# Performance work log

Measured on AMD Instinct MI355X. Metric: run time of the kernel, lower is better.

## Reference

```python
import jax, jax.numpy as jnp
import numpy as np

B, T, H = 32, 2048, 512
D = 2 * H  # bidirectional encoder feature dim


def setup_inputs() -> dict:
    key = jax.random.key(0)
    k1, k2, k3, k4, k5 = jax.random.split(key, 5)
    stdv = 1.0 / np.sqrt(H)
    return {
        "hidden": jax.random.normal(k1, (B, D), dtype=jnp.float32),
        "encoder_outputs": jax.random.normal(k2, (B, T, D), dtype=jnp.float32),
        "W_attn": jax.random.normal(k3, (H, 2 * D), dtype=jnp.float32) * stdv,
        "b_attn": jax.random.normal(k4, (H,), dtype=jnp.float32) * stdv,
        "v": jax.random.normal(k5, (H,), dtype=jnp.float32) * stdv,
    }


def reference(hidden, encoder_outputs, W_attn, b_attn, v):
    # The original per-timestep sliding-window loop recomputes a position-wise
    # Linear+tanh+dot whose value is independent of the window index, and
    # overlapping writes overwrite with identical values. The exact same math
    # is full additive attention over all T positions.
    d = encoder_outputs.shape[-1]
    Wh = W_attn[:, :d]   # acts on repeated decoder hidden state
    We = W_attn[:, d:]   # acts on encoder outputs
    # [B, H] ; avoids materializing the [B, T, 4H] concat
    hid_proj = jnp.einsum('bd,hd->bh', hidden, Wh)
    # [B, T, H]
    energy = jnp.tanh(jnp.einsum('btd,hd->bth', encoder_outputs, We)
                      + hid_proj[:, None, :] + b_attn)
    scores = jnp.einsum('bth,h->bt', energy, v)  # [B, T]
    return jax.nn.softmax(scores, axis=1)[:, None, :]  # [B, 1, T]
```

## Files before the change

### kernel.cpp

```cpp
#include <hip/hip_runtime.h>

#define Bv 32
#define Tv 2048
#define Hv 512
#define Dv 1024

using bf16x8 = __attribute__((ext_vector_type(8))) __bf16;
using bf16x4 = __attribute__((ext_vector_type(4))) __bf16;
using f32x4  = __attribute__((ext_vector_type(4))) float;

__global__ void swizzle_we(const float* __restrict__ W, bf16x8* __restrict__ We_sw) {
    int g = blockIdx.x * 256 + threadIdx.x;
    int h = g >> 7;
    int d = (g & 127) * 8;
    const float* src = W + h * (2 * Dv) + Dv + d;
    float4 f0 = *(const float4*)src;
    float4 f1 = *(const float4*)(src + 4);
    bf16x8 o;
    o[0] = (__bf16)f0.x; o[1] = (__bf16)f0.y; o[2] = (__bf16)f0.z; o[3] = (__bf16)f0.w;
    o[4] = (__bf16)f1.x; o[5] = (__bf16)f1.y; o[6] = (__bf16)f1.z; o[7] = (__bf16)f1.w;
    int s = ((h >> 4) * 32 + (d >> 5)) * 64 + (((d >> 3) & 3) << 4) + (h & 15);
    We_sw[s] = o;
}

__global__ void hid_proj_kernel(const float* __restrict__ hidden,
                                const float* __restrict__ W,
                                const float* __restrict__ b_attn,
                                float* __restrict__ hp) {
    int h   = blockIdx.x;
    int tid = threadIdx.x;
    float4 wh = ((const float4*)(W + h * (2 * Dv)))[tid];
    __shared__ float red[4][Bv];
    int lane = tid & 63, w = tid >> 6;
    for (int b = 0; b < Bv; ++b) {
        float4 x = ((const float4*)(hidden + b * Dv))[tid];
        float p = wh.x * x.x + wh.y * x.y + wh.z * x.z + wh.w * x.w;
#pragma unroll
        for (int m = 1; m < 64; m <<= 1) p += __shfl_xor(p, m);
        if (lane == 0) red[w][b] = p;
    }
    __syncthreads();
    if (tid < Bv)
        hp[tid * Hv + h] = red[0][tid] + red[1][tid] + red[2][tid] + red[3][tid] + b_attn[h];
}

__device__ __forceinline__ float fast_tanh(float x) {
    float xc = fminf(fmaxf(x, -9.0f), 9.0f);
    float e  = __expf(2.0f * xc);
    return 1.0f - 2.0f / (e + 1.0f);
}

__global__ __launch_bounds__(512) void attn_main(
    const float* __restrict__ enc, const bf16x8* __restrict__ Bg,
    const float* __restrict__ hp, const float* __restrict__ vvec,
    float* __restrict__ scores)
{
    __shared__ __align__(16) __bf16 Abuf[2][64 * 72];
    __shared__ float redbuf[8][64];

    const int tid   = threadIdx.x;
    const int lane  = tid & 63;
    const int w     = tid >> 6;
    const int row0  = blockIdx.x * 64;
    const int batch = row0 >> 11;

    const int srow = tid >> 3;
    const int sd0  = (tid & 7) * 4;
    const float* gA = enc + (row0 + srow) * Dv + sd0;
    __bf16* lw0 = &Abuf[0][srow * 72 + sd0];

    const bf16x8* Bptr = Bg + (w * 4 * 32) * 64 + lane;

    f32x4 acc[4][4];
#pragma unroll
    for (int i = 0; i < 4; ++i)
#pragma unroll
        for (int j = 0; j < 4; ++j)
            acc[i][j] = (f32x4){0.f, 0.f, 0.f, 0.f};

    float4 f0 = *(const float4*)gA;
    float4 f1 = *(const float4*)(gA + 32);
    bf16x8 Bc[2][4];
#pragma unroll
    for (int ktl = 0; ktl < 2; ++ktl)
#pragma unroll
        for (int j = 0; j < 4; ++j)
            Bc[ktl][j] = Bptr[(j * 32 + ktl) * 64];

    const int arow  = lane & 15;
    const int acol8 = (lane >> 4) * 8;

    for (int kc = 0; kc < 16; ++kc) {
        __bf16* p = lw0 + (kc & 1) * (64 * 72);
        bf16x4 o0, o1;
        o0[0] = (__bf16)f0.x; o0[1] = (__bf16)f0.y; o0[2] = (__bf16)f0.z; o0[3] = (__bf16)f0.w;
        o1[0] = (__bf16)f1.x; o1[1] = (__bf16)f1.y; o1[2] = (__bf16)f1.z; o1[3] = (__bf16)f1.w;
        *(bf16x4*)p        = o0;
        *(bf16x4*)(p + 32) = o1;
        if (kc < 15) {
            f0 = *(const float4*)(gA + (kc + 1) * 64);
            f1 = *(const float4*)(gA + (kc + 1) * 64 + 32);
        }
        __syncthreads();

        bf16x8 Bn[2][4];
        if (kc < 15) {
#pragma unroll
            for (int ktl = 0; ktl < 2; ++ktl)
#pragma unroll
                for (int j = 0; j < 4; ++j)
                    Bn[ktl][j] = Bptr[(j * 32 + (kc + 1) * 2 + ktl) * 64];
        }

        const __bf16* rb = &Abuf[kc & 1][0];
#pragma unroll
        for (int ktl = 0; ktl < 2; ++ktl) {
            bf16x8 a0 = *(const bf16x8*)(rb + (0 * 16 + arow) * 72 + ktl * 32 + acol8);
            bf16x8 a1 = *(const bf16x8*)(rb + (1 * 16 + arow) * 72 + ktl * 32 + acol8);
            bf16x8 a2 = *(const bf16x8*)(rb + (2 * 16 + arow) * 72 + ktl * 32 + acol8);
            bf16x8 a3 = *(const bf16x8*)(rb + (3 * 16 + arow) * 72 + ktl * 32 + acol8);
#pragma unroll
            for (int j = 0; j < 4; ++j) {
                acc[0][j] = __builtin_amdgcn_mfma_f32_16x16x32_bf16(a0, Bc[ktl][j], acc[0][j], 0, 0, 0);
                acc[1][j] = __builtin_amdgcn_mfma_f32_16x16x32_bf16(a1, Bc[ktl][j], acc[1][j], 0, 0, 0);
                acc[2][j] = __builtin_amdgcn_mfma_f32_16x16x32_bf16(a2, Bc[ktl][j], acc[2][j], 0, 0, 0);
                acc[3][j] = __builtin_amdgcn_mfma_f32_16x16x32_bf16(a3, Bc[ktl][j], acc[3][j], 0, 0, 0);
            }
        }
#pragma unroll
        for (int ktl = 0; ktl < 2; ++ktl)
#pragma unroll
            for (int j = 0; j < 4; ++j)
                Bc[ktl][j] = Bn[ktl][j];
    }

    float hpv[4], vv[4];
#pragma unroll
    for (int j = 0; j < 4; ++j) {
        int n  = w * 64 + j * 16 + (lane & 15);
        hpv[j] = hp[batch * Hv + n];
        vv[j]  = vvec[n];
    }
    const int qrow = (lane >> 4) * 4;
#pragma unroll
    for (int mt = 0; mt < 4; ++mt)
#pragma unroll
        for (int r = 0; r < 4; ++r) {
            float p = 0.f;
#pragma unroll
            for (int j = 0; j < 4; ++j)
                p += vv[j] * fast_tanh(acc[mt][j][r] + hpv[j]);
            p += __shfl_xor(p, 1);
            p += __shfl_xor(p, 2);
            p += __shfl_xor(p, 4);
            p += __shfl_xor(p, 8);
            if ((lane & 15) == 0)
                redbuf[w][mt * 16 + qrow + r] = p;
        }
    __syncthreads();
    if (tid < 64) {
        float s = 0.f;
#pragma unroll
        for (int ww = 0; ww < 8; ++ww) s += redbuf[ww][tid];
        scores[row0 + tid] = s;
    }
}

__global__ void softmax_kernel(const float* __restrict__ scores, float* __restrict__ out) {
    int b   = blockIdx.x;
    int tid = threadIdx.x;
    const float* s = scores + b * Tv;
    float local[8];
    float m = -1e30f;
#pragma unroll
    for (int i = 0; i < 8; ++i) { local[i] = s[tid + i * 256]; m = fmaxf(m, local[i]); }
    __shared__ float red[4];
    int lane = tid & 63, w = tid >> 6;
#pragma unroll
    for (int x = 1; x < 64; x <<= 1) m = fmaxf(m, __shfl_xor(m, x));
    if (lane == 0) red[w] = m;
    __syncthreads();
    m = fmaxf(fmaxf(red[0], red[1]), fmaxf(red[2], red[3]));
    float sum = 0.f;
#pragma unroll
    for (int i = 0; i < 8; ++i) { local[i] = expf(local[i] - m); sum += local[i]; }
#pragma unroll
    for (int x = 1; x < 64; x <<= 1) sum += __shfl_xor(sum, x);
    __syncthreads();
    if (lane == 0) red[w] = sum;
    __syncthreads();
    sum = red[0] + red[1] + red[2] + red[3];
    float inv = 1.0f / sum;
#pragma unroll
    for (int i = 0; i < 8; ++i) out[b * Tv + tid + i * 256] = local[i] * inv;
}

extern "C" void kernel_launch(void* const* d_in, const int* in_sizes, int n_in,
                              void* d_out, int out_size, void* d_ws, size_t ws_size,
                              hipStream_t stream) {
    const float* hidden = (const float*)d_in[0];
    const float* enc    = (const float*)d_in[1];
    const float* W      = (const float*)d_in[2];
    const float* b_attn = (const float*)d_in[3];
    const float* v      = (const float*)d_in[4];
    float* out = (float*)d_out;

    char* ws = (char*)d_ws;
    bf16x8* We_sw = (bf16x8*)ws;
    float*  hp    = (float*)(ws + (1 << 20));
    float*  sc    = (float*)(ws + (1 << 20) + (1 << 16));

    swizzle_we<<<256, 256, 0, stream>>>(W, We_sw);
    hid_proj_kernel<<<Hv, 256, 0, stream>>>(hidden, W, b_attn, hp);
    attn_main<<<(Bv * Tv) / 64, 512, 0, stream>>>(enc, We_sw, hp, v, sc);
    softmax_kernel<<<Bv, 256, 0, stream>>>(sc, out);
}
```

Before: 443.2 us.

## Fuse prep kernels, swizzle A tile in LDS, deepen global prefetch, set occupancy

Merges the W_e swizzle and hidden-projection kernels into one launch to save a kernel launch. In the main GEMM, the A tile is stored in LDS in an MFMA-fragment-swizzled layout so each lane reads one contiguous bf16x8. Global loads of encoder rows are prefetched two k-chunks ahead, and the k loop is fully unrolled. The block barrier becomes a raw s_waitcnt lgkmcnt(0)+s_barrier, and launch_bounds asks for 2 blocks per CU, which caps register use and risks spills.

```diff
diff --git a/kernel.cpp b/kernel.cpp
--- a/kernel.cpp
+++ b/kernel.cpp
@@ -9,39 +9,38 @@
 using bf16x4 = __attribute__((ext_vector_type(4))) __bf16;
 using f32x4  = __attribute__((ext_vector_type(4))) float;
 
-__global__ void swizzle_we(const float* __restrict__ W, bf16x8* __restrict__ We_sw) {
-    int g = blockIdx.x * 256 + threadIdx.x;
-    int h = g >> 7;
-    int d = (g & 127) * 8;
-    const float* src = W + h * (2 * Dv) + Dv + d;
-    float4 f0 = *(const float4*)src;
-    float4 f1 = *(const float4*)(src + 4);
-    bf16x8 o;
-    o[0] = (__bf16)f0.x; o[1] = (__bf16)f0.y; o[2] = (__bf16)f0.z; o[3] = (__bf16)f0.w;
-    o[4] = (__bf16)f1.x; o[5] = (__bf16)f1.y; o[6] = (__bf16)f1.z; o[7] = (__bf16)f1.w;
-    int s = ((h >> 4) * 32 + (d >> 5)) * 64 + (((d >> 3) & 3) << 4) + (h & 15);
-    We_sw[s] = o;
-}
-
-__global__ void hid_proj_kernel(const float* __restrict__ hidden,
-                                const float* __restrict__ W,
-                                const float* __restrict__ b_attn,
-                                float* __restrict__ hp) {
-    int h   = blockIdx.x;
-    int tid = threadIdx.x;
-    float4 wh = ((const float4*)(W + h * (2 * Dv)))[tid];
-    __shared__ float red[4][Bv];
-    int lane = tid & 63, w = tid >> 6;
-    for (int b = 0; b < Bv; ++b) {
-        float4 x = ((const float4*)(hidden + b * Dv))[tid];
-        float p = wh.x * x.x + wh.y * x.y + wh.z * x.z + wh.w * x.w;
-#pragma unroll
-        for (int m = 1; m < 64; m <<= 1) p += __shfl_xor(p, m);
-        if (lane == 0) red[w][b] = p;
-    }
-    __syncthreads();
-    if (tid < Bv)
-        hp[tid * Hv + h] = red[0][tid] + red[1][tid] + red[2][tid] + red[3][tid] + b_attn[h];
+__global__ void prep_kernel(const float* __restrict__ W, bf16x8* __restrict__ We_sw,
+                            const float* __restrict__ hidden,
+                            const float* __restrict__ b_attn, float* __restrict__ hp) {
+    if (blockIdx.x < 256) {
+        int g = blockIdx.x * 256 + threadIdx.x;
+        int h = g >> 7;
+        int d = (g & 127) * 8;
+        const float* src = W + h * (2 * Dv) + Dv + d;
+        float4 f0 = *(const float4*)src;
+        float4 f1 = *(const float4*)(src + 4);
+        bf16x8 o;
+        o[0] = (__bf16)f0.x; o[1] = (__bf16)f0.y; o[2] = (__bf16)f0.z; o[3] = (__bf16)f0.w;
+        o[4] = (__bf16)f1.x; o[5] = (__bf16)f1.y; o[6] = (__bf16)f1.z; o[7] = (__bf16)f1.w;
+        int s = ((h >> 4) * 32 + (d >> 5)) * 64 + (((d >> 3) & 3) << 4) + (h & 15);
+        We_sw[s] = o;
+    } else {
+        int h   = blockIdx.x - 256;
+        int tid = threadIdx.x;
+        float4 wh = ((const float4*)(W + h * (2 * Dv)))[tid];
+        __shared__ float red[4][Bv];
+        int lane = tid & 63, w = tid >> 6;
+        for (int b = 0; b < Bv; ++b) {
+            float4 x = ((const float4*)(hidden + b * Dv))[tid];
+            float p = wh.x * x.x + wh.y * x.y + wh.z * x.z + wh.w * x.w;
+#pragma unroll
+            for (int m = 1; m < 64; m <<= 1) p += __shfl_xor(p, m);
+            if (lane == 0) red[w][b] = p;
+        }
+        __syncthreads();
+        if (tid < Bv)
+            hp[tid * Hv + h] = red[0][tid] + red[1][tid] + red[2][tid] + red[3][tid] + b_attn[h];
+    }
 }
 
 __device__ __forceinline__ float fast_tanh(float x) {
@@ -50,12 +49,12 @@
     return 1.0f - 2.0f / (e + 1.0f);
 }
 
-__global__ __launch_bounds__(512) void attn_main(
+__global__ __launch_bounds__(512, 2) void attn_main(
     const float* __restrict__ enc, const bf16x8* __restrict__ Bg,
     const float* __restrict__ hp, const float* __restrict__ vvec,
     float* __restrict__ scores)
 {
-    __shared__ __align__(16) __bf16 Abuf[2][64 * 72];
+    __shared__ bf16x8 Abuf[2][512];
     __shared__ float redbuf[8][64];
 
     const int tid   = threadIdx.x;
@@ -64,12 +63,14 @@
     const int row0  = blockIdx.x * 64;
     const int batch = row0 >> 11;
 
-    const int srow = tid >> 3;
-    const int sd0  = (tid & 7) * 4;
-    const float* gA = enc + (row0 + srow) * Dv + sd0;
-    __bf16* lw0 = &Abuf[0][srow * 72 + sd0];
-
-    const bf16x8* Bptr = Bg + (w * 4 * 32) * 64 + lane;
+    const int srow = tid >> 4;
+    const int kk   = (tid & 15) * 4;
+    const float* gA = enc + (row0 + srow) * Dv + kk;
+    const int mt0  = srow >> 4, aa = srow & 15;
+    const int ktl0 = kk >> 5,  qq = (kk >> 3) & 3, jb = kk & 7;
+    __bf16* lw = (__bf16*)(&Abuf[0][0]) + (((mt0 * 2 + ktl0) * 64 + aa * 4 + qq) << 3) + jb;
+
+    const bf16x8* Bptr = Bg + (w * 128) * 64 + lane;
 
     f32x4 acc[4][4];
 #pragma unroll
@@ -78,8 +79,10 @@
         for (int j = 0; j < 4; ++j)
             acc[i][j] = (f32x4){0.f, 0.f, 0.f, 0.f};
 
-    float4 f0 = *(const float4*)gA;
-    float4 f1 = *(const float4*)(gA + 32);
+    float4 fa0 = *(const float4*)gA;
+    float4 fa1 = *(const float4*)(gA + 32 * Dv);
+    float4 fb0 = *(const float4*)(gA + 64);
+    float4 fb1 = *(const float4*)(gA + 32 * Dv + 64);
     bf16x8 Bc[2][4];
 #pragma unroll
     for (int ktl = 0; ktl < 2; ++ktl)
@@ -87,22 +90,24 @@
         for (int j = 0; j < 4; ++j)
             Bc[ktl][j] = Bptr[(j * 32 + ktl) * 64];
 
-    const int arow  = lane & 15;
-    const int acol8 = (lane >> 4) * 8;
-
+    const int rsl = ((lane & 15) << 2) + (lane >> 4);
+
+#pragma unroll
     for (int kc = 0; kc < 16; ++kc) {
-        __bf16* p = lw0 + (kc & 1) * (64 * 72);
+        __bf16* p = lw + (kc & 1) * 4096;
         bf16x4 o0, o1;
-        o0[0] = (__bf16)f0.x; o0[1] = (__bf16)f0.y; o0[2] = (__bf16)f0.z; o0[3] = (__bf16)f0.w;
-        o1[0] = (__bf16)f1.x; o1[1] = (__bf16)f1.y; o1[2] = (__bf16)f1.z; o1[3] = (__bf16)f1.w;
-        *(bf16x4*)p        = o0;
-        *(bf16x4*)(p + 32) = o1;
-        if (kc < 15) {
-            f0 = *(const float4*)(gA + (kc + 1) * 64);
-            f1 = *(const float4*)(gA + (kc + 1) * 64 + 32);
-        }
-        __syncthreads();
-
+        o0[0] = (__bf16)fa0.x; o0[1] = (__bf16)fa0.y; o0[2] = (__bf16)fa0.z; o0[3] = (__bf16)fa0.w;
+        o1[0] = (__bf16)fa1.x; o1[1] = (__bf16)fa1.y; o1[2] = (__bf16)fa1.z; o1[3] = (__bf16)fa1.w;
+        *(bf16x4*)p          = o0;
+        *(bf16x4*)(p + 2048) = o1;
+
+        asm volatile("s_waitcnt lgkmcnt(0)\n\ts_barrier" ::: "memory");
+
+        fa0 = fb0; fa1 = fb1;
+        if (kc < 14) {
+            fb0 = *(const float4*)(gA + (kc + 2) * 64);
+            fb1 = *(const float4*)(gA + 32 * Dv + (kc + 2) * 64);
+        }
         bf16x8 Bn[2][4];
         if (kc < 15) {
 #pragma unroll
@@ -112,13 +117,13 @@
                     Bn[ktl][j] = Bptr[(j * 32 + (kc + 1) * 2 + ktl) * 64];
         }
 
-        const __bf16* rb = &Abuf[kc & 1][0];
+        const bf16x8* rb = &Abuf[kc & 1][0];
 #pragma unroll
         for (int ktl = 0; ktl < 2; ++ktl) {
-            bf16x8 a0 = *(const bf16x8*)(rb + (0 * 16 + arow) * 72 + ktl * 32 + acol8);
-            bf16x8 a1 = *(const bf16x8*)(rb + (1 * 16 + arow) * 72 + ktl * 32 + acol8);
-            bf16x8 a2 = *(const bf16x8*)(rb + (2 * 16 + arow) * 72 + ktl * 32 + acol8);
-            bf16x8 a3 = *(const bf16x8*)(rb + (3 * 16 + arow) * 72 + ktl * 32 + acol8);
+            bf16x8 a0 = rb[(0 * 2 + ktl) * 64 + rsl];
+            bf16x8 a1 = rb[(1 * 2 + ktl) * 64 + rsl];
+            bf16x8 a2 = rb[(2 * 2 + ktl) * 64 + rsl];
+            bf16x8 a3 = rb[(3 * 2 + ktl) * 64 + rsl];
 #pragma unroll
             for (int j = 0; j < 4; ++j) {
                 acc[0][j] = __builtin_amdgcn_mfma_f32_16x16x32_bf16(a0, Bc[ktl][j], acc[0][j], 0, 0, 0);
@@ -210,8 +215,7 @@
     float*  hp    = (float*)(ws + (1 << 20));
     float*  sc    = (float*)(ws + (1 << 20) + (1 << 16));
 
-    swizzle_we<<<256, 256, 0, stream>>>(W, We_sw);
-    hid_proj_kernel<<<Hv, 256, 0, stream>>>(hidden, W, b_attn, hp);
+    prep_kernel<<<768, 256, 0, stream>>>(W, We_sw, hidden, b_attn, hp);
     attn_main<<<(Bv * Tv) / 64, 512, 0, stream>>>(enc, We_sw, hp, v, sc);
     softmax_kernel<<<Bv, 256, 0, stream>>>(sc, out);
 }
```

After: 445.3 us. About the same (+0.5%).

## Merge prep kernels and deepen A-tile prefetch in attention GEMM

Applied to the files above, without the earlier changes.

Merges the weight swizzle and hidden projection kernels into one launch to cut a kernel launch. In the main GEMM kernel it prefetches encoder rows two K-chunks ahead instead of one, and loads B fragments just in time rather than double-buffering them in registers. It also replaces __syncthreads with a raw LDS-wait plus barrier, fully unrolls the K loop, and requests 4 blocks per CU via launch bounds. The aim is to hide global-load latency and lower register pressure for higher occupancy, at the risk of exposed B-load latency or spills.

```diff
diff --git a/kernel.cpp b/kernel.cpp
--- a/kernel.cpp
+++ b/kernel.cpp
@@ -9,39 +9,38 @@
 using bf16x4 = __attribute__((ext_vector_type(4))) __bf16;
 using f32x4  = __attribute__((ext_vector_type(4))) float;
 
-__global__ void swizzle_we(const float* __restrict__ W, bf16x8* __restrict__ We_sw) {
-    int g = blockIdx.x * 256 + threadIdx.x;
-    int h = g >> 7;
-    int d = (g & 127) * 8;
-    const float* src = W + h * (2 * Dv) + Dv + d;
-    float4 f0 = *(const float4*)src;
-    float4 f1 = *(const float4*)(src + 4);
-    bf16x8 o;
-    o[0] = (__bf16)f0.x; o[1] = (__bf16)f0.y; o[2] = (__bf16)f0.z; o[3] = (__bf16)f0.w;
-    o[4] = (__bf16)f1.x; o[5] = (__bf16)f1.y; o[6] = (__bf16)f1.z; o[7] = (__bf16)f1.w;
-    int s = ((h >> 4) * 32 + (d >> 5)) * 64 + (((d >> 3) & 3) << 4) + (h & 15);
-    We_sw[s] = o;
-}
-
-__global__ void hid_proj_kernel(const float* __restrict__ hidden,
-                                const float* __restrict__ W,
-                                const float* __restrict__ b_attn,
-                                float* __restrict__ hp) {
-    int h   = blockIdx.x;
-    int tid = threadIdx.x;
-    float4 wh = ((const float4*)(W + h * (2 * Dv)))[tid];
-    __shared__ float red[4][Bv];
-    int lane = tid & 63, w = tid >> 6;
-    for (int b = 0; b < Bv; ++b) {
-        float4 x = ((const float4*)(hidden + b * Dv))[tid];
-        float p = wh.x * x.x + wh.y * x.y + wh.z * x.z + wh.w * x.w;
-#pragma unroll
-        for (int m = 1; m < 64; m <<= 1) p += __shfl_xor(p, m);
-        if (lane == 0) red[w][b] = p;
-    }
-    __syncthreads();
-    if (tid < Bv)
-        hp[tid * Hv + h] = red[0][tid] + red[1][tid] + red[2][tid] + red[3][tid] + b_attn[h];
+__global__ void prep_kernel(const float* __restrict__ W, bf16x8* __restrict__ We_sw,
+                            const float* __restrict__ hidden,
+                            const float* __restrict__ b_attn, float* __restrict__ hp) {
+    if (blockIdx.x < 256) {
+        int g = blockIdx.x * 256 + threadIdx.x;
+        int h = g >> 7;
+        int d = (g & 127) * 8;
+        const float* src = W + h * (2 * Dv) + Dv + d;
+        float4 f0 = *(const float4*)src;
+        float4 f1 = *(const float4*)(src + 4);
+        bf16x8 o;
+        o[0] = (__bf16)f0.x; o[1] = (__bf16)f0.y; o[2] = (__bf16)f0.z; o[3] = (__bf16)f0.w;
+        o[4] = (__bf16)f1.x; o[5] = (__bf16)f1.y; o[6] = (__bf16)f1.z; o[7] = (__bf16)f1.w;
+        int s = ((h >> 4) * 32 + (d >> 5)) * 64 + (((d >> 3) & 3) << 4) + (h & 15);
+        We_sw[s] = o;
+    } else {
+        int h   = blockIdx.x - 256;
+        int tid = threadIdx.x;
+        float4 wh = ((const float4*)(W + h * (2 * Dv)))[tid];
+        __shared__ float red[4][Bv];
+        int lane = tid & 63, w = tid >> 6;
+        for (int b = 0; b < Bv; ++b) {
+            float4 x = ((const float4*)(hidden + b * Dv))[tid];
+            float p = wh.x * x.x + wh.y * x.y + wh.z * x.z + wh.w * x.w;
+#pragma unroll
+            for (int m = 1; m < 64; m <<= 1) p += __shfl_xor(p, m);
+            if (lane == 0) red[w][b] = p;
+        }
+        __syncthreads();
+        if (tid < Bv)
+            hp[tid * Hv + h] = red[0][tid] + red[1][tid] + red[2][tid] + red[3][tid] + b_attn[h];
+    }
 }
 
 __device__ __forceinline__ float fast_tanh(float x) {
@@ -50,7 +49,7 @@
     return 1.0f - 2.0f / (e + 1.0f);
 }
 
-__global__ __launch_bounds__(512) void attn_main(
+__global__ __launch_bounds__(512, 4) void attn_main(
     const float* __restrict__ enc, const bf16x8* __restrict__ Bg,
     const float* __restrict__ hp, const float* __restrict__ vvec,
     float* __restrict__ scores)
@@ -69,7 +68,7 @@
     const float* gA = enc + (row0 + srow) * Dv + sd0;
     __bf16* lw0 = &Abuf[0][srow * 72 + sd0];
 
-    const bf16x8* Bptr = Bg + (w * 4 * 32) * 64 + lane;
+    const bf16x8* Bptr = Bg + (w * 128) * 64 + lane;
 
     f32x4 acc[4][4];
 #pragma unroll
@@ -78,60 +77,59 @@
         for (int j = 0; j < 4; ++j)
             acc[i][j] = (f32x4){0.f, 0.f, 0.f, 0.f};
 
-    float4 f0 = *(const float4*)gA;
-    float4 f1 = *(const float4*)(gA + 32);
-    bf16x8 Bc[2][4];
-#pragma unroll
-    for (int ktl = 0; ktl < 2; ++ktl)
-#pragma unroll
-        for (int j = 0; j < 4; ++j)
-            Bc[ktl][j] = Bptr[(j * 32 + ktl) * 64];
+    float4 fa0 = *(const float4*)gA;
+    float4 fa1 = *(const float4*)(gA + 32);
+    float4 fb0 = *(const float4*)(gA + 64);
+    float4 fb1 = *(const float4*)(gA + 96);
 
     const int arow  = lane & 15;
     const int acol8 = (lane >> 4) * 8;
 
+#pragma unroll
     for (int kc = 0; kc < 16; ++kc) {
         __bf16* p = lw0 + (kc & 1) * (64 * 72);
         bf16x4 o0, o1;
-        o0[0] = (__bf16)f0.x; o0[1] = (__bf16)f0.y; o0[2] = (__bf16)f0.z; o0[3] = (__bf16)f0.w;
-        o1[0] = (__bf16)f1.x; o1[1] = (__bf16)f1.y; o1[2] = (__bf16)f1.z; o1[3] = (__bf16)f1.w;
+        o0[0] = (__bf16)fa0.x; o0[1] = (__bf16)fa0.y; o0[2] = (__bf16)fa0.z; o0[3] = (__bf16)fa0.w;
+        o1[0] = (__bf16)fa1.x; o1[1] = (__bf16)fa1.y; o1[2] = (__bf16)fa1.z; o1[3] = (__bf16)fa1.w;
         *(bf16x4*)p        = o0;
         *(bf16x4*)(p + 32) = o1;
-        if (kc < 15) {
-            f0 = *(const float4*)(gA + (kc + 1) * 64);
-            f1 = *(const float4*)(gA + (kc + 1) * 64 + 32);
-        }
-        __syncthreads();
-
-        bf16x8 Bn[2][4];
-        if (kc < 15) {
-#pragma unroll
-            for (int ktl = 0; ktl < 2; ++ktl)
-#pragma unroll
-                for (int j = 0; j < 4; ++j)
-                    Bn[ktl][j] = Bptr[(j * 32 + (kc + 1) * 2 + ktl) * 64];
+
+        asm volatile("s_waitcnt lgkmcnt(0)\n\ts_barrier" ::: "memory");
+
+        fa0 = fb0; fa1 = fb1;
+        if (kc < 14) {
+            fb0 = *(const float4*)(gA + (kc + 2) * 64);
+            fb1 = *(const float4*)(gA + (kc + 2) * 64 + 32);
         }
 
         const __bf16* rb = &Abuf[kc & 1][0];
 #pragma unroll
         for (int ktl = 0; ktl < 2; ++ktl) {
+            bf16x8 b0 = Bptr[(0 * 32 + kc * 2 + ktl) * 64];
+            bf16x8 b1 = Bptr[(1 * 32 + kc * 2 + ktl) * 64];
+            bf16x8 b2 = Bptr[(2 * 32 + kc * 2 + ktl) * 64];
+            bf16x8 b3 = Bptr[(3 * 32 + kc * 2 + ktl) * 64];
             bf16x8 a0 = *(const bf16x8*)(rb + (0 * 16 + arow) * 72 + ktl * 32 + acol8);
             bf16x8 a1 = *(const bf16x8*)(rb + (1 * 16 + arow) * 72 + ktl * 32 + acol8);
             bf16x8 a2 = *(const bf16x8*)(rb + (2 * 16 + arow) * 72 + ktl * 32 + acol8);
             bf16x8 a3 = *(const bf16x8*)(rb + (3 * 16 + arow) * 72 + ktl * 32 + acol8);
-#pragma unroll
-            for (int j = 0; j < 4; ++j) {
-                acc[0][j] = __builtin_amdgcn_mfma_f32_16x16x32_bf16(a0, Bc[ktl][j], acc[0][j], 0, 0, 0);
-                acc[1][j] = __builtin_amdgcn_mfma_f32_16x16x32_bf16(a1, Bc[ktl][j], acc[1][j], 0, 0, 0);
-                acc[2][j] = __builtin_amdgcn_mfma_f32_16x16x32_bf16(a2, Bc[ktl][j], acc[2][j], 0, 0, 0);
-                acc[3][j] = __builtin_amdgcn_mfma_f32_16x16x32_bf16(a3, Bc[ktl][j], acc[3][j], 0, 0, 0);
-            }
-        }
-#pragma unroll
-        for (int ktl = 0; ktl < 2; ++ktl)
-#pragma unroll
-            for (int j = 0; j < 4; ++j)
-                Bc[ktl][j] = Bn[ktl][j];
+            acc[0][0] = __builtin_amdgcn_mfma_f32_16x16x32_bf16(a0, b0, acc[0][0], 0, 0, 0);
+            acc[1][0] = __builtin_amdgcn_mfma_f32_16x16x32_bf16(a1, b0, acc[1][0], 0, 0, 0);
+            acc[2][0] = __builtin_amdgcn_mfma_f32_16x16x32_bf16(a2, b0, acc[2][0], 0, 0, 0);
+            acc[3][0] = __builtin_amdgcn_mfma_f32_16x16x32_bf16(a3, b0, acc[3][0], 0, 0, 0);
+            acc[0][1] = __builtin_amdgcn_mfma_f32_16x16x32_bf16(a0, b1, acc[0][1], 0, 0, 0);
+            acc[1][1] = __builtin_amdgcn_mfma_f32_16x16x32_bf16(a1, b1, acc[1][1], 0, 0, 0);
+            acc[2][1] = __builtin_amdgcn_mfma_f32_16x16x32_bf16(a2, b1, acc[2][1], 0, 0, 0);
+            acc[3][1] = __builtin_amdgcn_mfma_f32_16x16x32_bf16(a3, b1, acc[3][1], 0, 0, 0);
+            acc[0][2] = __builtin_amdgcn_mfma_f32_16x16x32_bf16(a0, b2, acc[0][2], 0, 0, 0);
+            acc[1][2] = __builtin_amdgcn_mfma_f32_16x16x32_bf16(a1, b2, acc[1][2], 0, 0, 0);
+            acc[2][2] = __builtin_amdgcn_mfma_f32_16x16x32_bf16(a2, b2, acc[2][2], 0, 0, 0);
+            acc[3][2] = __builtin_amdgcn_mfma_f32_16x16x32_bf16(a3, b2, acc[3][2], 0, 0, 0);
+            acc[0][3] = __builtin_amdgcn_mfma_f32_16x16x32_bf16(a0, b3, acc[0][3], 0, 0, 0);
+            acc[1][3] = __builtin_amdgcn_mfma_f32_16x16x32_bf16(a1, b3, acc[1][3], 0, 0, 0);
+            acc[2][3] = __builtin_amdgcn_mfma_f32_16x16x32_bf16(a2, b3, acc[2][3], 0, 0, 0);
+            acc[3][3] = __builtin_amdgcn_mfma_f32_16x16x32_bf16(a3, b3, acc[3][3], 0, 0, 0);
+        }
     }
 
     float hpv[4], vv[4];
@@ -210,8 +208,7 @@
     float*  hp    = (float*)(ws + (1 << 20));
     float*  sc    = (float*)(ws + (1 << 20) + (1 << 16));
 
-    swizzle_we<<<256, 256, 0, stream>>>(W, We_sw);
-    hid_proj_kernel<<<Hv, 256, 0, stream>>>(hidden, W, b_attn, hp);
+    prep_kernel<<<768, 256, 0, stream>>>(W, We_sw, hidden, b_attn, hp);
     attn_main<<<(Bv * Tv) / 64, 512, 0, stream>>>(enc, We_sw, hp, v, sc);
     softmax_kernel<<<Bv, 256, 0, stream>>>(sc, out);
 }
```

Measured after the change: 456.7 us. 1.03x slower.
